# Kernel optimization log

Measured on AMD Instinct MI355X. Metric: run time of the kernel, lower is better.

Reference implementation:

```python
import jax, jax.numpy as jnp
import numpy as np
from jax import lax
from jax.scipy.special import logsumexp

V, H, L, C, B, T = 30000, 512, 2, 9, 128, 256


def setup_inputs() -> dict:
    key = jax.random.key(0)
    ks = jax.random.split(key, 14)
    k = 1.0 / np.sqrt(H)
    u = lambda kk, shp, s: jax.random.uniform(kk, shp, jnp.float32, -s, s)
    embed = jax.random.normal(ks[0], (V, H), jnp.float32) * 0.5
    embed = embed.at[0].set(0.0)  # padding_idx=0
    w_ih_l0 = u(ks[1], (2, 4 * H, H), k)      # [dir, 4H, in]
    w_hh_l0 = u(ks[2], (2, 4 * H, H), k)
    b_l0 = u(ks[3], (2, 4 * H), k)            # b_ih + b_hh combined
    w_ih_l1 = u(ks[4], (2, 4 * H, 2 * H), k)  # layer-1 input is 2H (bidir concat)
    w_hh_l1 = u(ks[5], (2, 4 * H, H), k)
    b_l1 = u(ks[6], (2, 4 * H), k)
    kc = 1.0 / np.sqrt(2 * H)
    cls_w = u(ks[7], (C, 2 * H), kc)
    cls_b = u(ks[8], (C,), kc)
    crf_start = u(ks[9], (C,), 0.1)
    crf_end = u(ks[10], (C,), 0.1)
    crf_trans = u(ks[11], (C, C), 0.1)
    x = jax.random.randint(ks[12], (B, T), 0, V)
    y = jax.random.randint(ks[13], (B, T), 0, C)
    return dict(x=x, y=y, embed=embed, w_ih_l0=w_ih_l0, w_hh_l0=w_hh_l0, b_l0=b_l0,
                w_ih_l1=w_ih_l1, w_hh_l1=w_hh_l1, b_l1=b_l1, cls_w=cls_w, cls_b=cls_b,
                crf_start=crf_start, crf_end=crf_end, crf_trans=crf_trans)


def _lstm_dir(xs, w_ih, w_hh, b):
    # xs: [T, B, Din] -> hidden states [T, B, H]
    Bn, Hn = xs.shape[1], w_hh.shape[-1]
    pre = jnp.einsum('tbd,gd->tbg', xs, w_ih) + b  # hoist input GEMM out of scan

    def step(carry, zt):
        h, c = carry
        z = zt + h @ w_hh.T
        i, f, g, o = jnp.split(z, 4, axis=-1)
        c = jax.nn.sigmoid(f) * c + jax.nn.sigmoid(i) * jnp.tanh(g)
        h = jax.nn.sigmoid(o) * jnp.tanh(c)
        return (h, c), h

    init = (jnp.zeros((Bn, Hn), xs.dtype), jnp.zeros((Bn, Hn), xs.dtype))
    _, hs = lax.scan(step, init, pre)
    return hs


def _bilstm_layer(xs, w_ih, w_hh, b):
    hf = _lstm_dir(xs, w_ih[0], w_hh[0], b[0])
    hb = _lstm_dir(xs[::-1], w_ih[1], w_hh[1], b[1])[::-1]
    return jnp.concatenate([hf, hb], axis=-1)  # [T, B, 2H]


def reference(x, y, embed, w_ih_l0, w_hh_l0, b_l0, w_ih_l1, w_hh_l1, b_l1,
              cls_w, cls_b, crf_start, crf_end, crf_trans):
    mask = y > -1                              # [B, T] (all True here)
    # Embedding with max_norm=1 (rows renormalized to L2 norm <= 1 at lookup)
    emb = embed[x]                             # [B, T, H]
    nrm = jnp.linalg.norm(emb, axis=-1, keepdims=True)
    emb = emb * jnp.where(nrm > 1.0, 1.0 / (nrm + 1e-7), 1.0)

    xs = emb.transpose(1, 0, 2)                # [T, B, H]
    hs = _bilstm_layer(xs, w_ih_l0, w_hh_l0, b_l0)
    hs = _bilstm_layer(hs, w_ih_l1, w_hh_l1, b_l1)
    emissions = jnp.einsum('tbh,ch->tbc', hs, cls_w) + cls_b  # [T, B, C]

    tags = jnp.maximum(y, 0).T                 # [T, B]
    mT = mask.T                                # [T, B] bool
    mF = mT.astype(emissions.dtype)
    bidx = jnp.arange(B)

    # ---- numerator: score of gold path ----
    em_tag = jnp.take_along_axis(emissions, tags[:, :, None], axis=-1)[..., 0]  # [T, B]
    trans_sc = crf_trans[tags[:-1], tags[1:]]  # [T-1, B]
    score = crf_start[tags[0]] + em_tag[0]
    score = score + jnp.sum((trans_sc + em_tag[1:]) * mF[1:], axis=0)
    seq_ends = jnp.sum(mT, axis=0) - 1         # [B]
    last_tags = tags[seq_ends, bidx]
    score = score + crf_end[last_tags]

    # ---- denominator: forward algorithm ----
    alpha0 = crf_start + emissions[0]          # [B, C]

    def den_step(alpha, inp):
        e_t, m_t = inp
        nxt = logsumexp(alpha[:, :, None] + crf_trans[None] + e_t[:, None, :], axis=1)
        return jnp.where(m_t[:, None], nxt, alpha), None

    alpha, _ = lax.scan(den_step, alpha0, (emissions[1:], mT[1:]))
    denom = logsumexp(alpha + crf_end, axis=1)

    llh = score - denom
    return -jnp.mean(llh)
```

## Files before the change

kernel.cpp:

```cpp
#include <hip/hip_runtime.h>
#include <hip/hip_bf16.h>

#define VV 30000
#define HH 512
#define NC 9
#define BB 128
#define TT 256
#define GG 2048
#define TB (TT*BB)

using short8 = __attribute__((ext_vector_type(8))) short;
using f32x4  = __attribute__((ext_vector_type(4))) float;

__device__ inline float bf2f(unsigned short u){
    union { unsigned int i; float f; } v; v.i = ((unsigned int)u) << 16; return v.f;
}
__device__ inline unsigned short f2bf(float f){
    union { unsigned int i; float f; } v; v.f = f;
    unsigned int x = v.i;
    unsigned int r = (x + 0x7fffu + ((x >> 16) & 1u)) >> 16;
    return (unsigned short)r;
}
__device__ inline float sigm(float x){
    if (x >= 0.f){ return 1.f / (1.f + __expf(-x)); }
    float e = __expf(x); return e / (1.f + e);
}
__device__ inline float tanh_f(float x){
    float ax = fabsf(x);
    float e = __expf(-2.f * ax);
    float t = (1.f - e) / (1.f + e);
    return copysignf(t, x);
}

__global__ void castbf(const float* __restrict__ in, unsigned short* __restrict__ out, int n){
    int i = blockIdx.x * blockDim.x + threadIdx.x;
    if (i < n) out[i] = f2bf(in[i]);
}

__global__ __launch_bounds__(256) void embed_k(const int* __restrict__ x,
                                               const float* __restrict__ embed,
                                               unsigned short* __restrict__ xs){
    int wid  = (int)((blockIdx.x * blockDim.x + threadIdx.x) >> 6);
    int lane = threadIdx.x & 63;
    if (wid >= TB) return;
    int t = wid >> 7, b = wid & 127;
    int tok = x[b * TT + t];
    const float4* e = (const float4*)(embed + (size_t)tok * HH);
    float4 v0 = e[lane], v1 = e[lane + 64];
    float ss = v0.x*v0.x + v0.y*v0.y + v0.z*v0.z + v0.w*v0.w
             + v1.x*v1.x + v1.y*v1.y + v1.z*v1.z + v1.w*v1.w;
    #pragma unroll
    for (int off = 32; off > 0; off >>= 1) ss += __shfl_xor(ss, off, 64);
    float nrm = sqrtf(ss);
    float sc = (nrm > 1.f) ? 1.f / (nrm + 1e-7f) : 1.f;
    unsigned short* dst = xs + (size_t)wid * HH;
    ushort4 o0, o1;
    o0.x = f2bf(v0.x * sc); o0.y = f2bf(v0.y * sc); o0.z = f2bf(v0.z * sc); o0.w = f2bf(v0.w * sc);
    o1.x = f2bf(v1.x * sc); o1.y = f2bf(v1.y * sc); o1.z = f2bf(v1.z * sc); o1.w = f2bf(v1.w * sc);
    ((ushort4*)dst)[lane]      = o0;
    ((ushort4*)dst)[lane + 64] = o1;
}

__global__ __launch_bounds__(256) void gemm2(const unsigned short* __restrict__ A0,
                                             const unsigned short* __restrict__ A1,
                                             const unsigned short* __restrict__ Wb_,
                                             const float* __restrict__ bias,
                                             unsigned short* __restrict__ Cout,
                                             int K, int CH){
    const int dz = blockIdx.z;
    const unsigned short* A  = dz ? A1 : A0;
    const unsigned short* W  = Wb_ + (size_t)dz * GG * K;
    const float*          bd = bias + dz * GG;
    unsigned short*       C  = Cout + (size_t)dz * CH * BB * GG;

    __shared__ __align__(16) unsigned short smem[16384];

    const int tid  = threadIdx.x;
    const int lane = tid & 63;
    const int wv   = tid >> 6;
    const int l15  = lane & 15, quad = lane >> 4;
    const int mw   = (wv >> 1) * 64;
    const int nw   = (wv & 1) * 64;

    const int nwg   = gridDim.x * gridDim.y;
    const int chunk = nwg >> 3;
    const int id    = blockIdx.x + gridDim.x * blockIdx.y;
    const int nid   = (id & 7) * chunk + (id >> 3);
    const int m0    = (nid % gridDim.x) * 128;
    const int n0    = (nid / gridDim.x) * 128;

    const int srow = lane >> 2;
    const int scol = (lane & 3) * 8;
    const int c0 = wv * 2, c1 = wv * 2 + 1;
    const unsigned short* gA0 = A + (size_t)(m0 + c0 * 16 + srow) * K + scol;
    const unsigned short* gA1 = A + (size_t)(m0 + c1 * 16 + srow) * K + scol;
    const unsigned short* gB0 = W + (size_t)(n0 + c0 * 16 + srow) * K + scol;
    const unsigned short* gB1 = W + (size_t)(n0 + c1 * 16 + srow) * K + scol;

    f32x4 acc[4][4];
    #pragma unroll
    for (int i = 0; i < 4; i++)
        #pragma unroll
        for (int j = 0; j < 4; j++){ acc[i][j][0]=0.f; acc[i][j][1]=0.f; acc[i][j][2]=0.f; acc[i][j][3]=0.f; }

    #define STAGE(bufi, kko)                                                                              \
        do {                                                                                              \
            __builtin_amdgcn_global_load_lds((const __attribute__((address_space(1))) void*)(gA0 + (kko)),\
                (__attribute__((address_space(3))) void*)(smem + (bufi) * 4096 + c0 * 512), 16, 0, 0);    \
            __builtin_amdgcn_global_load_lds((const __attribute__((address_space(1))) void*)(gA1 + (kko)),\
                (__attribute__((address_space(3))) void*)(smem + (bufi) * 4096 + c1 * 512), 16, 0, 0);    \
            __builtin_amdgcn_global_load_lds((const __attribute__((address_space(1))) void*)(gB0 + (kko)),\
                (__attribute__((address_space(3))) void*)(smem + 8192 + (bufi) * 4096 + c0 * 512), 16, 0, 0);\
            __builtin_amdgcn_global_load_lds((const __attribute__((address_space(1))) void*)(gB1 + (kko)),\
                (__attribute__((address_space(3))) void*)(smem + 8192 + (bufi) * 4096 + c1 * 512), 16, 0, 0);\
        } while (0)

    const int nk = K >> 5;
    STAGE(0, 0);
    for (int t = 0; t < nk; ++t){
        const int buf = t & 1;
        const bool more = (t + 1 < nk);
        if (more){
            STAGE((t + 1) & 1, (t + 1) << 5);
            __builtin_amdgcn_sched_barrier(0);
            asm volatile("s_waitcnt vmcnt(4)" ::: "memory");
        } else {
            __builtin_amdgcn_sched_barrier(0);
            asm volatile("s_waitcnt vmcnt(0)" ::: "memory");
        }
        __builtin_amdgcn_s_barrier();
        __builtin_amdgcn_sched_barrier(0);

        short8 a[4], b[4];
        #pragma unroll
        for (int i = 0; i < 4; i++) a[i] = *(const short8*)&smem[(size_t)buf * 4096 + (mw + i * 16 + l15) * 32 + quad * 8];
        #pragma unroll
        for (int j = 0; j < 4; j++) b[j] = *(const short8*)&smem[8192 + (size_t)buf * 4096 + (nw + j * 16 + l15) * 32 + quad * 8];
        #pragma unroll
        for (int i = 0; i < 4; i++)
            #pragma unroll
            for (int j = 0; j < 4; j++)
                acc[i][j] = __builtin_amdgcn_mfma_f32_16x16x32_bf16(a[i], b[j], acc[i][j], 0, 0, 0);

        __builtin_amdgcn_sched_barrier(0);
        __builtin_amdgcn_s_barrier();
        __builtin_amdgcn_sched_barrier(0);
    }
    #undef STAGE

    #pragma unroll
    for (int i = 0; i < 4; i++){
        #pragma unroll
        for (int j = 0; j < 4; j++){
            const int ncol = nw + j * 16 + l15;
            const float bn = bd[n0 + ncol];
            #pragma unroll
            for (int r = 0; r < 4; r++){
                const int mrow = mw + i * 16 + quad * 4 + r;
                smem[mrow * 128 + ncol] = f2bf(acc[i][j][r] + bn);
            }
        }
    }
    __syncthreads();
    #pragma unroll
    for (int it = 0; it < 8; it++){
        const int ch  = it * 256 + tid;
        const int row = ch >> 4;
        const int col = (ch & 15) * 8;
        *(short8*)(C + (size_t)(m0 + row) * GG + n0 + col) = *(const short8*)&smem[row * 128 + col];
    }
}

__global__ __launch_bounds__(256) void lstm_seq(const unsigned short* __restrict__ preC,
                                                const unsigned short* __restrict__ whh,
                                                unsigned short* __restrict__ hA,
                                                unsigned short* __restrict__ hB,
                                                float* __restrict__ cstate,
                                                unsigned short* __restrict__ hs_out,
                                                const float* __restrict__ cw,
                                                float* __restrict__ em,
                                                int t0, int nsteps, int CH,
                                                unsigned int* __restrict__ bar){
    __shared__ unsigned short w_s[4][16][520];
    __shared__ unsigned short htile[64][20];
    __shared__ float cw_s[NC][16];

    const int tid  = threadIdx.x;
    const int lane = tid & 63;
    const int wv   = tid >> 6;
    const int l15  = lane & 15, quad = lane >> 4;
    const int bx   = blockIdx.x;
    const int grp  = bx & 3;
    const int d    = grp >> 1;
    const int mh   = grp & 1;
    const int jc   = bx >> 2;
    const int m0   = mh * 64;

    {
        const unsigned short* wbase = whh + (size_t)d * GG * HH;
        #pragma unroll
        for (int it = 0; it < 16; it++){
            int idx  = it * 256 + tid;
            int row  = idx >> 6;
            int col8 = idx & 63;
            int g2 = row >> 4, j2 = row & 15;
            short8 v = *(const short8*)(wbase + (size_t)(g2 * 512 + jc * 16 + j2) * HH + col8 * 8);
            *(short8*)&w_s[g2][j2][col8 * 8] = v;
        }
    }
    if (cw != nullptr && tid < NC * 16){
        int c = tid >> 4, j = tid & 15;
        cw_s[c][j] = cw[(size_t)c * 1024 + d * 512 + jc * 16 + j];
    }

    float csreg[4];
    #pragma unroll
    for (int rr = 0; rr < 4; rr++){
        const int gm = m0 + wv * 16 + quad * 4 + rr;
        csreg[rr] = cstate[((size_t)d * BB + gm) * HH + jc * 16 + l15];
    }

    unsigned short pf[4][4];
    {
        const int time0 = d ? (TT - 1 - t0) : t0;
        const int slot0 = time0 & (CH - 1);
        const unsigned short* p0 = preC + (((size_t)(d * CH + slot0)) * BB + (m0 + wv * 16 + quad * 4)) * GG + jc * 16 + l15;
        #pragma unroll
        for (int rr = 0; rr < 4; rr++)
            #pragma unroll
            for (int g = 0; g < 4; g++)
                pf[rr][g] = p0[(size_t)rr * GG + g * 512];
    }
    __syncthreads();

    const size_t slabU = (size_t)grp * 8192;
    unsigned int* myFl  = bar + (((size_t)grp * 4 + wv) * 32 + jc) * 16;
    const unsigned int* pollFl = bar + (((size_t)grp * 4 + wv) * 32 + (lane & 31)) * 16;

    const int rowu = (wv * 16 + l15) * 4 + (quad & 1) * 2;
    const int jq   = quad >> 1;

    unsigned short pfN[4][4];

    for (int ls = 0; ls < nsteps; ls++){
        const int tt   = t0 + ls;
        const unsigned long long* srcU = (const unsigned long long*)((tt & 1) ? hB : hA) + slabU;
        unsigned long long*       dstU = (unsigned long long*)((tt & 1) ? hA : hB) + slabU + (size_t)jc * 256;

        if (ls > 0){
            const unsigned int tgt = (unsigned int)ls;
            while (__hip_atomic_load(pollFl, __ATOMIC_RELAXED, __HIP_MEMORY_SCOPE_AGENT) < tgt)
                __builtin_amdgcn_s_sleep(1);
            __builtin_amdgcn_fence(__ATOMIC_ACQUIRE, "workgroup");
            #pragma unroll
            for (int rr = 0; rr < 4; rr++)
                #pragma unroll
                for (int g = 0; g < 4; g++)
                    pf[rr][g] = pfN[rr][g];
        }

        unsigned long long afr[16][2];
        #pragma unroll
        for (int kk = 0; kk < 16; kk++){
            const unsigned long long* p = srcU + (size_t)(2 * kk + jq) * 256 + rowu;
            afr[kk][0] = __hip_atomic_load(p,     __ATOMIC_RELAXED, __HIP_MEMORY_SCOPE_AGENT);
            afr[kk][1] = __hip_atomic_load(p + 1, __ATOMIC_RELAXED, __HIP_MEMORY_SCOPE_AGENT);
        }

        f32x4 acc[4];
        #pragma unroll
        for (int g = 0; g < 4; g++){ acc[g][0]=0.f; acc[g][1]=0.f; acc[g][2]=0.f; acc[g][3]=0.f; }
        #pragma unroll
        for (int kk = 0; kk < 16; kk++){
            union { unsigned long long u[2]; short8 s; } cv;
            cv.u[0] = afr[kk][0]; cv.u[1] = afr[kk][1];
            const short8 a = cv.s;
            #pragma unroll
            for (int g = 0; g < 4; g++){
                short8 b = *(const short8*)&w_s[g][l15][kk * 32 + quad * 8];
                acc[g] = __builtin_amdgcn_mfma_f32_16x16x32_bf16(a, b, acc[g], 0, 0, 0);
            }
        }

        #pragma unroll
        for (int rr = 0; rr < 4; rr++){
            const int lr = wv * 16 + quad * 4 + rr;
            const float zi = acc[0][rr] + bf2f(pf[rr][0]);
            const float zf = acc[1][rr] + bf2f(pf[rr][1]);
            const float zg = acc[2][rr] + bf2f(pf[rr][2]);
            const float zo = acc[3][rr] + bf2f(pf[rr][3]);
            float cs = sigm(zf) * csreg[rr] + sigm(zi) * tanh_f(zg);
            csreg[rr] = cs;
            htile[lr][l15] = f2bf(sigm(zo) * tanh_f(cs));
        }
        const int trowL = lane >> 2;
        const unsigned long long hv8 = *(const unsigned long long*)&htile[wv * 16 + trowL][(lane & 3) * 4];

        __hip_atomic_store(dstU + wv * 64 + lane, hv8, __ATOMIC_RELAXED, __HIP_MEMORY_SCOPE_AGENT);
        asm volatile("s_waitcnt vmcnt(0)" ::: "memory");
        __hip_atomic_store(myFl, (unsigned int)(ls + 1), __ATOMIC_RELAXED, __HIP_MEMORY_SCOPE_AGENT);

        const int time = d ? (TT - 1 - tt) : tt;
        const bool more = (ls + 1 < nsteps);

        if (more){
            const int tt1 = tt + 1;
            const int time1 = d ? (TT - 1 - tt1) : tt1;
            const int slot1 = time1 & (CH - 1);
            const unsigned short* p1 = preC + (((size_t)(d * CH + slot1)) * BB + (m0 + wv * 16 + quad * 4)) * GG + jc * 16 + l15;
            #pragma unroll
            for (int rr = 0; rr < 4; rr++)
                #pragma unroll
                for (int g = 0; g < 4; g++)
                    pfN[rr][g] = p1[(size_t)rr * GG + g * 512];
        }

        if (cw == nullptr){
            *(unsigned long long*)(hs_out + ((size_t)time * BB + m0 + wv * 16 + trowL) * (2 * HH) + d * HH + jc * 16 + (lane & 3) * 4) = hv8;
        } else {
            const int part = lane & 3;
            float hvv[4];
            #pragma unroll
            for (int k = 0; k < 4; k++) hvv[k] = bf2f((unsigned short)(hv8 >> (16 * k)));
            float p[NC];
            #pragma unroll
            for (int c = 0; c < NC; c++){
                float s = 0.f;
                #pragma unroll
                for (int k = 0; k < 4; k++) s += hvv[k] * cw_s[c][part * 4 + k];
                p[c] = s;
            }
            #pragma unroll
            for (int c = 0; c < NC; c++){
                p[c] += __shfl_xor(p[c], 1, 64);
                p[c] += __shfl_xor(p[c], 2, 64);
            }
            if (part == 0){
                float* emr = em + ((size_t)time * BB + m0 + wv * 16 + trowL) * NC;
                #pragma unroll
                for (int c = 0; c < NC; c++) atomicAdd(emr + c, p[c]);
            }
        }
    }

    #pragma unroll
    for (int rr = 0; rr < 4; rr++){
        const int gm = m0 + wv * 16 + quad * 4 + rr;
        cstate[((size_t)d * BB + gm) * HH + jc * 16 + l15] = csreg[rr];
    }
}

__global__ void eminit(const float* __restrict__ cb, float* __restrict__ em){
    int i = blockIdx.x * blockDim.x + threadIdx.x;
    if (i < TB * NC) em[i] = cb[i % NC];
}

__global__ __launch_bounds__(64) void crf_k(const int* __restrict__ y,
                                            const float* __restrict__ em,
                                            const float* __restrict__ cstart,
                                            const float* __restrict__ cend,
                                            const float* __restrict__ ctr,
                                            float* __restrict__ llh){
    int b = blockIdx.x;
    int lane = threadIdx.x;

    float sp = 0.f; int cnt = 0;
    for (int t = lane; t < TT; t += 64){
        int yt = y[b * TT + t];
        bool mk = (yt > -1);
        cnt += mk ? 1 : 0;
        if (t >= 1 && mk){
            int yp  = y[b * TT + t - 1];
            int tag  = yt > 0 ? yt : 0;
            int tagp = yp > 0 ? yp : 0;
            sp += ctr[tagp * NC + tag] + em[((size_t)t * BB + b) * NC + tag];
        }
    }
    #pragma unroll
    for (int off = 32; off > 0; off >>= 1){
        sp  += __shfl_xor(sp, off, 64);
        cnt += __shfl_xor(cnt, off, 64);
    }

    float trc[NC];
    #pragma unroll
    for (int cc2 = 0; cc2 < NC; cc2++) trc[cc2] = 0.f;
    if (lane < NC){
        #pragma unroll
        for (int cc2 = 0; cc2 < NC; cc2++) trc[cc2] = ctr[cc2 * NC + lane];
    }
    float alpha = -1e30f;
    if (lane < NC) alpha = cstart[lane] + em[(size_t)b * NC + lane];

    for (int t = 1; t < TT; t++){
        int yt = y[b * TT + t];
        bool mk = (yt > -1);
        float e = (lane < NC) ? em[((size_t)t * BB + b) * NC + lane] : 0.f;
        float v[NC]; float mx = -1e30f;
        #pragma unroll
        for (int cc2 = 0; cc2 < NC; cc2++){
            float ac = __shfl(alpha, cc2, 64);
            v[cc2] = ac + trc[cc2];
            mx = fmaxf(mx, v[cc2]);
        }
        float s = 0.f;
        #pragma unroll
        for (int cc2 = 0; cc2 < NC; cc2++) s += __expf(v[cc2] - mx);
        float nxt = mx + __logf(s) + e;
        if (mk && lane < NC) alpha = nxt;
    }

    float val = (lane < NC) ? (alpha + cend[lane]) : -1e30f;
    float mx = -1e30f;
    #pragma unroll
    for (int cc2 = 0; cc2 < NC; cc2++) mx = fmaxf(mx, __shfl(val, cc2, 64));
    float s = 0.f;
    #pragma unroll
    for (int cc2 = 0; cc2 < NC; cc2++) s += __expf(__shfl(val, cc2, 64) - mx);
    float denom = mx + __logf(s);

    if (lane == 0){
        int y0 = y[b * TT];
        int tag0 = y0 > 0 ? y0 : 0;
        int se = cnt - 1;
        if (se < 0) se = 0;
        int yl = y[b * TT + se];
        int tagl = yl > 0 ? yl : 0;
        float score = sp + cstart[tag0] + em[(size_t)b * NC + tag0] + cend[tagl];
        llh[b] = score - denom;
    }
}

__global__ void final_k(const float* __restrict__ llh, float* __restrict__ out){
    __shared__ float sm[128];
    int i = threadIdx.x;
    sm[i] = llh[i];
    __syncthreads();
    for (int s = 64; s > 0; s >>= 1){
        if (i < s) sm[i] += sm[i + s];
        __syncthreads();
    }
    if (i == 0) out[0] = -sm[0] / 128.f;
}

__global__ void sentinel_k(float* out, float v){ out[0] = v; }

extern "C" void kernel_launch(void* const* d_in, const int* in_sizes, int n_in,
                              void* d_out, int out_size, void* d_ws, size_t ws_size,
                              hipStream_t stream) {
    const int*   x     = (const int*)d_in[0];
    const int*   y     = (const int*)d_in[1];
    const float* embed = (const float*)d_in[2];
    const float* wih0  = (const float*)d_in[3];
    const float* whh0  = (const float*)d_in[4];
    const float* b0    = (const float*)d_in[5];
    const float* wih1  = (const float*)d_in[6];
    const float* whh1  = (const float*)d_in[7];
    const float* b1    = (const float*)d_in[8];
    const float* clsw  = (const float*)d_in[9];
    const float* clsb  = (const float*)d_in[10];
    const float* cst   = (const float*)d_in[11];
    const float* cen   = (const float*)d_in[12];
    const float* ctr   = (const float*)d_in[13];
    float* out = (float*)d_out;

    const size_t sz_w0   = (size_t)2 * GG * HH * 2;
    const size_t sz_w1   = (size_t)2 * GG * 1024 * 2;
    const size_t sz_xs   = (size_t)TB * HH * 2;
    const size_t sz_hs0  = (size_t)TB * 1024 * 2;
    const size_t sz_h    = (size_t)2 * BB * HH * 2;
    const size_t sz_c    = (size_t)2 * BB * HH * 4;
    const size_t sz_emis = (size_t)TB * NC * 4;
    const size_t sz_llh  = (size_t)BB * 4;
    const size_t sz_bar  = 32768;
    auto rup = [](size_t v){ return (v + 255) & ~(size_t)255; };
    size_t fixed = rup(sz_w0) * 3 + rup(sz_w1) + rup(sz_xs) + rup(sz_hs0)
                 + rup(sz_h) * 2 + rup(sz_c) + rup(sz_emis) + rup(sz_llh) + rup(sz_bar);

    const int cands[7] = {256, 128, 64, 32, 16, 8, 4};
    int CH = 0;
    for (int i = 0; i < 7; i++){
        size_t need = fixed + rup((size_t)2 * cands[i] * BB * GG * 2);
        if (need <= ws_size){ CH = cands[i]; break; }
    }
    if (CH == 0){
        sentinel_k<<<1, 1, 0, stream>>>(out, -(float)(ws_size >> 20));
        return;
    }

    char* ws = (char*)d_ws;
    size_t off = 0;
    auto alloc = [&](size_t bytes) -> void* {
        void* p = (void*)(ws + off);
        off += (bytes + 255) & ~(size_t)255;
        return p;
    };
    unsigned short* wih0b = (unsigned short*)alloc(sz_w0);
    unsigned short* whh0b = (unsigned short*)alloc(sz_w0);
    unsigned short* whh1b = (unsigned short*)alloc(sz_w0);
    unsigned short* wih1b = (unsigned short*)alloc(sz_w1);
    unsigned short* xs    = (unsigned short*)alloc(sz_xs);
    unsigned short* hs0   = (unsigned short*)alloc(sz_hs0);
    unsigned short* hA    = (unsigned short*)alloc(sz_h);
    unsigned short* hB    = (unsigned short*)alloc(sz_h);
    float*          cbuf  = (float*)alloc(sz_c);
    float*          emis  = (float*)alloc(sz_emis);
    float*          llh   = (float*)alloc(sz_llh);
    unsigned int*   bar   = (unsigned int*)alloc(sz_bar);
    unsigned short* preC  = (unsigned short*)alloc((size_t)2 * CH * BB * GG * 2);

    castbf<<<(2 * GG * HH + 255) / 256, 256, 0, stream>>>(wih0, wih0b, 2 * GG * HH);
    castbf<<<(2 * GG * HH + 255) / 256, 256, 0, stream>>>(whh0, whh0b, 2 * GG * HH);
    castbf<<<(2 * GG * 1024 + 255) / 256, 256, 0, stream>>>(wih1, wih1b, 2 * GG * 1024);
    castbf<<<(2 * GG * HH + 255) / 256, 256, 0, stream>>>(whh1, whh1b, 2 * GG * HH);

    embed_k<<<TB / 4, 256, 0, stream>>>(x, embed, xs);

    const int nch = TT / CH;

    (void)hipMemsetAsync(hA, 0, sz_h, stream);
    (void)hipMemsetAsync(cbuf, 0, sz_c, stream);
    for (int c = 0; c < nch; c++){
        int t0f = c * CH;
        int t0b = TT - (c + 1) * CH;
        gemm2<<<dim3(CH, GG / 128, 2), 256, 0, stream>>>(
            xs + (size_t)t0f * BB * HH, xs + (size_t)t0b * BB * HH,
            wih0b, b0, preC, HH, CH);
        (void)hipMemsetAsync(bar, 0, sz_bar, stream);
        lstm_seq<<<128, 256, 0, stream>>>(preC, whh0b, hA, hB, cbuf, hs0,
                                          nullptr, emis, c * CH, CH, CH, bar);
    }

    eminit<<<(TB * NC + 255) / 256, 256, 0, stream>>>(clsb, emis);

    (void)hipMemsetAsync(hA, 0, sz_h, stream);
    (void)hipMemsetAsync(cbuf, 0, sz_c, stream);
    for (int c = 0; c < nch; c++){
        int t0f = c * CH;
        int t0b = TT - (c + 1) * CH;
        gemm2<<<dim3(CH, GG / 128, 2), 256, 0, stream>>>(
            hs0 + (size_t)t0f * BB * 1024, hs0 + (size_t)t0b * BB * 1024,
            wih1b, b1, preC, 1024, CH);
        (void)hipMemsetAsync(bar, 0, sz_bar, stream);
        lstm_seq<<<128, 256, 0, stream>>>(preC, whh1b, hA, hB, cbuf, hs0,
                                          clsw, emis, c * CH, CH, CH, bar);
    }

    crf_k<<<BB, 64, 0, stream>>>(y, emis, cst, cen, ctr, llh);
    final_k<<<1, 128, 0, stream>>>(llh, out);
}
```

Before: 5.015 ms.

## Overlap next-chunk input GEMM with LSTM recurrence in a fused kernel

```diff
diff --git a/kernel.cpp b/kernel.cpp
--- a/kernel.cpp
+++ b/kernel.cpp
@@ -171,182 +171,300 @@
     }
 }
 
-__global__ __launch_bounds__(256) void lstm_seq(const unsigned short* __restrict__ preC,
-                                                const unsigned short* __restrict__ whh,
-                                                unsigned short* __restrict__ hA,
-                                                unsigned short* __restrict__ hB,
-                                                float* __restrict__ cstate,
-                                                unsigned short* __restrict__ hs_out,
-                                                const float* __restrict__ cw,
-                                                float* __restrict__ em,
-                                                int t0, int nsteps, int CH,
-                                                unsigned int* __restrict__ bar){
-    __shared__ unsigned short w_s[4][16][520];
-    __shared__ unsigned short htile[64][20];
-    __shared__ float cw_s[NC][16];
+__global__ __launch_bounds__(256) void lstm_fused(const unsigned short* __restrict__ preC,
+                                                  const unsigned short* __restrict__ whh,
+                                                  unsigned short* __restrict__ hA,
+                                                  unsigned short* __restrict__ hB,
+                                                  float* __restrict__ cstate,
+                                                  unsigned short* __restrict__ hs_out,
+                                                  const float* __restrict__ cw,
+                                                  float* __restrict__ em,
+                                                  int t0, int nsteps, int CH,
+                                                  unsigned int* __restrict__ bar,
+                                                  const unsigned short* __restrict__ An0,
+                                                  const unsigned short* __restrict__ An1,
+                                                  const unsigned short* __restrict__ Wi_,
+                                                  const float* __restrict__ bias,
+                                                  unsigned short* __restrict__ Cnext,
+                                                  int K, int njobs){
+    __shared__ __align__(16) unsigned char shm[69888];
 
     const int tid  = threadIdx.x;
+    const int bx   = blockIdx.x;
+
+    if (bx < 128){
+        unsigned short (*w_s)[16][520] = (unsigned short (*)[16][520])shm;
+        unsigned short (*htile)[20]    = (unsigned short (*)[20])(shm + 66560);
+        float (*cw_s)[16]              = (float (*)[16])(shm + 69120);
+
+        const int lane = tid & 63;
+        const int wv   = tid >> 6;
+        const int l15  = lane & 15, quad = lane >> 4;
+        const int grp  = bx & 3;
+        const int d    = grp >> 1;
+        const int mh   = grp & 1;
+        const int jc   = bx >> 2;
+        const int m0   = mh * 64;
+
+        {
+            const unsigned short* wbase = whh + (size_t)d * GG * HH;
+            #pragma unroll
+            for (int it = 0; it < 16; it++){
+                int idx  = it * 256 + tid;
+                int row  = idx >> 6;
+                int col8 = idx & 63;
+                int g2 = row >> 4, j2 = row & 15;
+                short8 v = *(const short8*)(wbase + (size_t)(g2 * 512 + jc * 16 + j2) * HH + col8 * 8);
+                *(short8*)&w_s[g2][j2][col8 * 8] = v;
+            }
+        }
+        if (cw != nullptr && tid < NC * 16){
+            int c = tid >> 4, j = tid & 15;
+            cw_s[c][j] = cw[(size_t)c * 1024 + d * 512 + jc * 16 + j];
+        }
+
+        float csreg[4];
+        #pragma unroll
+        for (int rr = 0; rr < 4; rr++){
+            const int gm = m0 + wv * 16 + quad * 4 + rr;
+            csreg[rr] = cstate[((size_t)d * BB + gm) * HH + jc * 16 + l15];
+        }
+
+        unsigned short pf[4][4];
+        {
+            const int time0 = d ? (TT - 1 - t0) : t0;
+            const int slot0 = time0 & (CH - 1);
+            const unsigned short* p0 = preC + (((size_t)(d * CH + slot0)) * BB + (m0 + wv * 16 + quad * 4)) * GG + jc * 16 + l15;
+            #pragma unroll
+            for (int rr = 0; rr < 4; rr++)
+                #pragma unroll
+                for (int g = 0; g < 4; g++)
+                    pf[rr][g] = p0[(size_t)rr * GG + g * 512];
+        }
+        __syncthreads();
+
+        const size_t slabU = (size_t)grp * 8192;
+        unsigned int* myFl  = bar + (((size_t)grp * 4 + wv) * 32 + jc) * 16;
+        const unsigned int* pollFl = bar + (((size_t)grp * 4 + wv) * 32 + (lane & 31)) * 16;
+
+        const int rowu = (wv * 16 + l15) * 4 + (quad & 1) * 2;
+        const int jq   = quad >> 1;
+
+        unsigned short pfN[4][4];
+
+        for (int ls = 0; ls < nsteps; ls++){
+            const int tt   = t0 + ls;
+            const unsigned long long* srcU = (const unsigned long long*)((tt & 1) ? hB : hA) + slabU;
+            unsigned long long*       dstU = (unsigned long long*)((tt & 1) ? hA : hB) + slabU + (size_t)jc * 256;
+
+            if (ls > 0){
+                const unsigned int tgt = (unsigned int)ls;
+                while (__hip_atomic_load(pollFl, __ATOMIC_RELAXED, __HIP_MEMORY_SCOPE_AGENT) < tgt)
+                    __builtin_amdgcn_s_sleep(1);
+                __builtin_amdgcn_fence(__ATOMIC_ACQUIRE, "workgroup");
+                #pragma unroll
+                for (int rr = 0; rr < 4; rr++)
+                    #pragma unroll
+                    for (int g = 0; g < 4; g++)
+                        pf[rr][g] = pfN[rr][g];
+            }
+
+            unsigned long long afr[16][2];
+            #pragma unroll
+            for (int kk = 0; kk < 16; kk++){
+                const unsigned long long* p = srcU + (size_t)(2 * kk + jq) * 256 + rowu;
+                afr[kk][0] = __hip_atomic_load(p,     __ATOMIC_RELAXED, __HIP_MEMORY_SCOPE_AGENT);
+                afr[kk][1] = __hip_atomic_load(p + 1, __ATOMIC_RELAXED, __HIP_MEMORY_SCOPE_AGENT);
+            }
+
+            f32x4 acc[4];
+            #pragma unroll
+            for (int g = 0; g < 4; g++){ acc[g][0]=0.f; acc[g][1]=0.f; acc[g][2]=0.f; acc[g][3]=0.f; }
+            #pragma unroll
+            for (int kk = 0; kk < 16; kk++){
+                union { unsigned long long u[2]; short8 s; } cv;
+                cv.u[0] = afr[kk][0]; cv.u[1] = afr[kk][1];
+                const short8 a = cv.s;
+                #pragma unroll
+                for (int g = 0; g < 4; g++){
+                    short8 b = *(const short8*)&w_s[g][l15][kk * 32 + quad * 8];
+                    acc[g] = __builtin_amdgcn_mfma_f32_16x16x32_bf16(a, b, acc[g], 0, 0, 0);
+                }
+            }
+
+            #pragma unroll
+            for (int rr = 0; rr < 4; rr++){
+                const int lr = wv * 16 + quad * 4 + rr;
+                const float zi = acc[0][rr] + bf2f(pf[rr][0]);
+                const float zf = acc[1][rr] + bf2f(pf[rr][1]);
+                const float zg = acc[2][rr] + bf2f(pf[rr][2]);
+                const float zo = acc[3][rr] + bf2f(pf[rr][3]);
+                float cs = sigm(zf) * csreg[rr] + sigm(zi) * tanh_f(zg);
+                csreg[rr] = cs;
+                htile[lr][l15] = f2bf(sigm(zo) * tanh_f(cs));
+            }
+            const int trowL = lane >> 2;
+            const unsigned long long hv8 = *(const unsigned long long*)&htile[wv * 16 + trowL][(lane & 3) * 4];
+
+            __hip_atomic_store(dstU + wv * 64 + lane, hv8, __ATOMIC_RELAXED, __HIP_MEMORY_SCOPE_AGENT);
+            asm volatile("s_waitcnt vmcnt(0)" ::: "memory");
+            __hip_atomic_store(myFl, (unsigned int)(ls + 1), __ATOMIC_RELAXED, __HIP_MEMORY_SCOPE_AGENT);
+
+            const int time = d ? (TT - 1 - tt) : tt;
+            const bool more = (ls + 1 < nsteps);
+
+            if (more){
+                const int tt1 = tt + 1;
+                const int time1 = d ? (TT - 1 - tt1) : tt1;
+                const int slot1 = time1 & (CH - 1);
+                const unsigned short* p1 = preC + (((size_t)(d * CH + slot1)) * BB + (m0 + wv * 16 + quad * 4)) * GG + jc * 16 + l15;
+                #pragma unroll
+                for (int rr = 0; rr < 4; rr++)
+                    #pragma unroll
+                    for (int g = 0; g < 4; g++)
+                        pfN[rr][g] = p1[(size_t)rr * GG + g * 512];
+            }
+
+            if (cw == nullptr){
+                *(unsigned long long*)(hs_out + ((size_t)time * BB + m0 + wv * 16 + trowL) * (2 * HH) + d * HH + jc * 16 + (lane & 3) * 4) = hv8;
+            } else {
+                const int part = lane & 3;
+                float hvv[4];
+                #pragma unroll
+                for (int k = 0; k < 4; k++) hvv[k] = bf2f((unsigned short)(hv8 >> (16 * k)));
+                float p[NC];
+                #pragma unroll
+                for (int c = 0; c < NC; c++){
+                    float s = 0.f;
+                    #pragma unroll
+                    for (int k = 0; k < 4; k++) s += hvv[k] * cw_s[c][part * 4 + k];
+                    p[c] = s;
+                }
+                #pragma unroll
+                for (int c = 0; c < NC; c++){
+                    p[c] += __shfl_xor(p[c], 1, 64);
+                    p[c] += __shfl_xor(p[c], 2, 64);
+                }
+                if (part == 0){
+                    float* emr = em + ((size_t)time * BB + m0 + wv * 16 + trowL) * NC;
+                    #pragma unroll
+                    for (int c = 0; c < NC; c++) atomicAdd(emr + c, p[c]);
+                }
+            }
+        }
+
+        #pragma unroll
+        for (int rr = 0; rr < 4; rr++){
+            const int gm = m0 + wv * 16 + quad * 4 + rr;
+            cstate[((size_t)d * BB + gm) * HH + jc * 16 + l15] = csreg[rr];
+        }
+        return;
+    }
+
+    if (An0 == nullptr) return;
+    unsigned short* smem = (unsigned short*)shm;
+
     const int lane = tid & 63;
     const int wv   = tid >> 6;
     const int l15  = lane & 15, quad = lane >> 4;
-    const int bx   = blockIdx.x;
-    const int grp  = bx & 3;
-    const int d    = grp >> 1;
-    const int mh   = grp & 1;
-    const int jc   = bx >> 2;
-    const int m0   = mh * 64;
-
-    {
-        const unsigned short* wbase = whh + (size_t)d * GG * HH;
-        #pragma unroll
-        for (int it = 0; it < 16; it++){
-            int idx  = it * 256 + tid;
-            int row  = idx >> 6;
-            int col8 = idx & 63;
-            int g2 = row >> 4, j2 = row & 15;
-            short8 v = *(const short8*)(wbase + (size_t)(g2 * 512 + jc * 16 + j2) * HH + col8 * 8);
-            *(short8*)&w_s[g2][j2][col8 * 8] = v;
-        }
-    }
-    if (cw != nullptr && tid < NC * 16){
-        int c = tid >> 4, j = tid & 15;
-        cw_s[c][j] = cw[(size_t)c * 1024 + d * 512 + jc * 16 + j];
-    }
-
-    float csreg[4];
-    #pragma unroll
-    for (int rr = 0; rr < 4; rr++){
-        const int gm = m0 + wv * 16 + quad * 4 + rr;
-        csreg[rr] = cstate[((size_t)d * BB + gm) * HH + jc * 16 + l15];
-    }
-
-    unsigned short pf[4][4];
-    {
-        const int time0 = d ? (TT - 1 - t0) : t0;
-        const int slot0 = time0 & (CH - 1);
-        const unsigned short* p0 = preC + (((size_t)(d * CH + slot0)) * BB + (m0 + wv * 16 + quad * 4)) * GG + jc * 16 + l15;
-        #pragma unroll
-        for (int rr = 0; rr < 4; rr++)
-            #pragma unroll
-            for (int g = 0; g < 4; g++)
-                pf[rr][g] = p0[(size_t)rr * GG + g * 512];
-    }
-    __syncthreads();
-
-    const size_t slabU = (size_t)grp * 8192;
-    unsigned int* myFl  = bar + (((size_t)grp * 4 + wv) * 32 + jc) * 16;
-    const unsigned int* pollFl = bar + (((size_t)grp * 4 + wv) * 32 + (lane & 31)) * 16;
-
-    const int rowu = (wv * 16 + l15) * 4 + (quad & 1) * 2;
-    const int jq   = quad >> 1;
-
-    unsigned short pfN[4][4];
-
-    for (int ls = 0; ls < nsteps; ls++){
-        const int tt   = t0 + ls;
-        const unsigned long long* srcU = (const unsigned long long*)((tt & 1) ? hB : hA) + slabU;
-        unsigned long long*       dstU = (unsigned long long*)((tt & 1) ? hA : hB) + slabU + (size_t)jc * 256;
-
-        if (ls > 0){
-            const unsigned int tgt = (unsigned int)ls;
-            while (__hip_atomic_load(pollFl, __ATOMIC_RELAXED, __HIP_MEMORY_SCOPE_AGENT) < tgt)
-                __builtin_amdgcn_s_sleep(1);
-            __builtin_amdgcn_fence(__ATOMIC_ACQUIRE, "workgroup");
-            #pragma unroll
-            for (int rr = 0; rr < 4; rr++)
-                #pragma unroll
-                for (int g = 0; g < 4; g++)
-                    pf[rr][g] = pfN[rr][g];
-        }
-
-        unsigned long long afr[16][2];
-        #pragma unroll
-        for (int kk = 0; kk < 16; kk++){
-            const unsigned long long* p = srcU + (size_t)(2 * kk + jq) * 256 + rowu;
-            afr[kk][0] = __hip_atomic_load(p,     __ATOMIC_RELAXED, __HIP_MEMORY_SCOPE_AGENT);
-            afr[kk][1] = __hip_atomic_load(p + 1, __ATOMIC_RELAXED, __HIP_MEMORY_SCOPE_AGENT);
-        }
-
-        f32x4 acc[4];
-        #pragma unroll
-        for (int g = 0; g < 4; g++){ acc[g][0]=0.f; acc[g][1]=0.f; acc[g][2]=0.f; acc[g][3]=0.f; }
-        #pragma unroll
-        for (int kk = 0; kk < 16; kk++){
-            union { unsigned long long u[2]; short8 s; } cv;
-            cv.u[0] = afr[kk][0]; cv.u[1] = afr[kk][1];
-            const short8 a = cv.s;
-            #pragma unroll
-            for (int g = 0; g < 4; g++){
-                short8 b = *(const short8*)&w_s[g][l15][kk * 32 + quad * 8];
-                acc[g] = __builtin_amdgcn_mfma_f32_16x16x32_bf16(a, b, acc[g], 0, 0, 0);
-            }
-        }
-
-        #pragma unroll
-        for (int rr = 0; rr < 4; rr++){
-            const int lr = wv * 16 + quad * 4 + rr;
-            const float zi = acc[0][rr] + bf2f(pf[rr][0]);
-            const float zf = acc[1][rr] + bf2f(pf[rr][1]);
-            const float zg = acc[2][rr] + bf2f(pf[rr][2]);
-            const float zo = acc[3][rr] + bf2f(pf[rr][3]);
-            float cs = sigm(zf) * csreg[rr] + sigm(zi) * tanh_f(zg);
-            csreg[rr] = cs;
-            htile[lr][l15] = f2bf(sigm(zo) * tanh_f(cs));
-        }
-        const int trowL = lane >> 2;
-        const unsigned long long hv8 = *(const unsigned long long*)&htile[wv * 16 + trowL][(lane & 3) * 4];
-
-        __hip_atomic_store(dstU + wv * 64 + lane, hv8, __ATOMIC_RELAXED, __HIP_MEMORY_SCOPE_AGENT);
-        asm volatile("s_waitcnt vmcnt(0)" ::: "memory");
-        __hip_atomic_store(myFl, (unsigned int)(ls + 1), __ATOMIC_RELAXED, __HIP_MEMORY_SCOPE_AGENT);
-
-        const int time = d ? (TT - 1 - tt) : tt;
-        const bool more = (ls + 1 < nsteps);
-
-        if (more){
-            const int tt1 = tt + 1;
-            const int time1 = d ? (TT - 1 - tt1) : tt1;
-            const int slot1 = time1 & (CH - 1);
-            const unsigned short* p1 = preC + (((size_t)(d * CH + slot1)) * BB + (m0 + wv * 16 + quad * 4)) * GG + jc * 16 + l15;
-            #pragma unroll
-            for (int rr = 0; rr < 4; rr++)
-                #pragma unroll
-                for (int g = 0; g < 4; g++)
-                    pfN[rr][g] = p1[(size_t)rr * GG + g * 512];
-        }
-
-        if (cw == nullptr){
-            *(unsigned long long*)(hs_out + ((size_t)time * BB + m0 + wv * 16 + trowL) * (2 * HH) + d * HH + jc * 16 + (lane & 3) * 4) = hv8;
-        } else {
-            const int part = lane & 3;
-            float hvv[4];
-            #pragma unroll
-            for (int k = 0; k < 4; k++) hvv[k] = bf2f((unsigned short)(hv8 >> (16 * k)));
-            float p[NC];
-            #pragma unroll
-            for (int c = 0; c < NC; c++){
-                float s = 0.f;
-                #pragma unroll
-                for (int k = 0; k < 4; k++) s += hvv[k] * cw_s[c][part * 4 + k];
-                p[c] = s;
-            }
-            #pragma unroll
-            for (int c = 0; c < NC; c++){
-                p[c] += __shfl_xor(p[c], 1, 64);
-                p[c] += __shfl_xor(p[c], 2, 64);
-            }
-            if (part == 0){
-                float* emr = em + ((size_t)time * BB + m0 + wv * 16 + trowL) * NC;
-                #pragma unroll
-                for (int c = 0; c < NC; c++) atomicAdd(emr + c, p[c]);
-            }
-        }
-    }
-
-    #pragma unroll
-    for (int rr = 0; rr < 4; rr++){
-        const int gm = m0 + wv * 16 + quad * 4 + rr;
-        cstate[((size_t)d * BB + gm) * HH + jc * 16 + l15] = csreg[rr];
+    const int mw   = (wv >> 1) * 64;
+    const int nw   = (wv & 1) * 64;
+    const int srow = lane >> 2;
+    const int scol = (lane & 3) * 8;
+    const int c0 = wv * 2, c1 = wv * 2 + 1;
+    const int nhb = (int)gridDim.x - 128;
+    const int CHn = nsteps;
+
+    for (int job = bx - 128; job < njobs; job += nhb){
+        const int xj  = job % CHn;
+        const int rem = job / CHn;
+        const int yj  = rem & 15;
+        const int dz  = rem >> 4;
+        const unsigned short* A  = dz ? An1 : An0;
+        const unsigned short* W  = Wi_ + (size_t)dz * GG * K;
+        const float*          bd = bias + dz * GG;
+        unsigned short*       C  = Cnext + (size_t)dz * CHn * BB * GG;
+        const int m0 = xj * 128;
+        const int n0 = yj * 128;
+
+        const unsigned short* gA0 = A + (size_t)(m0 + c0 * 16 + srow) * K + scol;
+        const unsigned short* gA1 = A + (size_t)(m0 + c1 * 16 + srow) * K + scol;
+        const unsigned short* gB0 = W + (size_t)(n0 + c0 * 16 + srow) * K + scol;
+        const unsigned short* gB1 = W + (size_t)(n0 + c1 * 16 + srow) * K + scol;
+
+        f32x4 acc[4][4];
+        #pragma unroll
+        for (int i = 0; i < 4; i++)
+            #pragma unroll
+            for (int j = 0; j < 4; j++){ acc[i][j][0]=0.f; acc[i][j][1]=0.f; acc[i][j][2]=0.f; acc[i][j][3]=0.f; }
+
+        #define HSTAGE(bufi, kko)                                                                             \
+            do {                                                                                              \
+                __builtin_amdgcn_global_load_lds((const __attribute__((address_space(1))) void*)(gA0 + (kko)),\
+                    (__attribute__((address_space(3))) void*)(smem + (bufi) * 4096 + c0 * 512), 16, 0, 0);    \
+                __builtin_amdgcn_global_load_lds((const __attribute__((address_space(1))) void*)(gA1 + (kko)),\
+                    (__attribute__((address_space(3))) void*)(smem + (bufi) * 4096 + c1 * 512), 16, 0, 0);    \
+                __builtin_amdgcn_global_load_lds((const __attribute__((address_space(1))) void*)(gB0 + (kko)),\
+                    (__attribute__((address_space(3))) void*)(smem + 8192 + (bufi) * 4096 + c0 * 512), 16, 0, 0);\
+                __builtin_amdgcn_global_load_lds((const __attribute__((address_space(1))) void*)(gB1 + (kko)),\
+                    (__attribute__((address_space(3))) void*)(smem + 8192 + (bufi) * 4096 + c1 * 512), 16, 0, 0);\
+            } while (0)
+
+        const int nk = K >> 5;
+        HSTAGE(0, 0);
+        for (int t = 0; t < nk; ++t){
+            const int buf = t & 1;
+            const bool more = (t + 1 < nk);
+            if (more){
+                HSTAGE((t + 1) & 1, (t + 1) << 5);
+                __builtin_amdgcn_sched_barrier(0);
+                asm volatile("s_waitcnt vmcnt(4)" ::: "memory");
+            } else {
+                __builtin_amdgcn_sched_barrier(0);
+                asm volatile("s_waitcnt vmcnt(0)" ::: "memory");
+            }
+            __builtin_amdgcn_s_barrier();
+            __builtin_amdgcn_sched_barrier(0);
+
+            short8 a[4], b[4];
+            #pragma unroll
+            for (int i = 0; i < 4; i++) a[i] = *(const short8*)&smem[(size_t)buf * 4096 + (mw + i * 16 + l15) * 32 + quad * 8];
+            #pragma unroll
+            for (int j = 0; j < 4; j++) b[j] = *(const short8*)&smem[8192 + (size_t)buf * 4096 + (nw + j * 16 + l15) * 32 + quad * 8];
+            #pragma unroll
+            for (int i = 0; i < 4; i++)
+                #pragma unroll
+                for (int j = 0; j < 4; j++)
+                    acc[i][j] = __builtin_amdgcn_mfma_f32_16x16x32_bf16(a[i], b[j], acc[i][j], 0, 0, 0);
+
+            __builtin_amdgcn_sched_barrier(0);
+            __builtin_amdgcn_s_barrier();
+            __builtin_amdgcn_sched_barrier(0);
+        }
+        #undef HSTAGE
+
+        #pragma unroll
+        for (int i = 0; i < 4; i++){
+            #pragma unroll
+            for (int j = 0; j < 4; j++){
+                const int ncol = nw + j * 16 + l15;
+                const float bn = bd[n0 + ncol];
+                #pragma unroll
+                for (int r = 0; r < 4; r++){
+                    const int mrow = mw + i * 16 + quad * 4 + r;
+                    smem[mrow * 128 + ncol] = f2bf(acc[i][j][r] + bn);
+                }
+            }
+        }
+        __syncthreads();
+        #pragma unroll
+        for (int it = 0; it < 8; it++){
+            const int ch  = it * 256 + tid;
+            const int row = ch >> 4;
+            const int col = (ch & 15) * 8;
+            *(short8*)(C + (size_t)(m0 + row) * GG + n0 + col) = *(const short8*)&smem[row * 128 + col];
+        }
+        __syncthreads();
     }
 }
 
@@ -477,16 +595,17 @@
     size_t fixed = rup(sz_w0) * 3 + rup(sz_w1) + rup(sz_xs) + rup(sz_hs0)
                  + rup(sz_h) * 2 + rup(sz_c) + rup(sz_emis) + rup(sz_llh) + rup(sz_bar);
 
-    const int cands[7] = {256, 128, 64, 32, 16, 8, 4};
+    const int cands[4] = {64, 32, 16, 8};
     int CH = 0;
-    for (int i = 0; i < 7; i++){
-        size_t need = fixed + rup((size_t)2 * cands[i] * BB * GG * 2);
-        if (need <= ws_size){ CH = cands[i]; break; }
+    for (int i = 0; i < 4; i++){
+        size_t par = (size_t)2 * cands[i] * BB * GG * 2;
+        if (fixed + 2 * rup(par) <= ws_size){ CH = cands[i]; break; }
     }
     if (CH == 0){
         sentinel_k<<<1, 1, 0, stream>>>(out, -(float)(ws_size >> 20));
         return;
     }
+    const size_t parSz = (size_t)2 * CH * BB * GG * 2;
 
     char* ws = (char*)d_ws;
     size_t off = 0;
@@ -507,7 +626,8 @@
     float*          emis  = (float*)alloc(sz_emis);
     float*          llh   = (float*)alloc(sz_llh);
     unsigned int*   bar   = (unsigned int*)alloc(sz_bar);
-    unsigned short* preC  = (unsigned short*)alloc((size_t)2 * CH * BB * GG * 2);
+    unsigned short* preC0 = (unsigned short*)alloc(parSz);
+    unsigned short* preC1 = (unsigned short*)alloc(parSz);
 
     castbf<<<(2 * GG * HH + 255) / 256, 256, 0, stream>>>(wih0, wih0b, 2 * GG * HH);
     castbf<<<(2 * GG * HH + 255) / 256, 256, 0, stream>>>(whh0, whh0b, 2 * GG * HH);
@@ -517,33 +637,40 @@
     embed_k<<<TB / 4, 256, 0, stream>>>(x, embed, xs);
 
     const int nch = TT / CH;
+    const int njobs = CH * 16 * 2;
+
+    eminit<<<(TB * NC + 255) / 256, 256, 0, stream>>>(clsb, emis);
 
     (void)hipMemsetAsync(hA, 0, sz_h, stream);
     (void)hipMemsetAsync(cbuf, 0, sz_c, stream);
+    gemm2<<<dim3(CH, GG / 128, 2), 256, 0, stream>>>(
+        xs, xs + (size_t)(TT - CH) * BB * HH, wih0b, b0, preC0, HH, CH);
     for (int c = 0; c < nch; c++){
-        int t0f = c * CH;
-        int t0b = TT - (c + 1) * CH;
-        gemm2<<<dim3(CH, GG / 128, 2), 256, 0, stream>>>(
-            xs + (size_t)t0f * BB * HH, xs + (size_t)t0b * BB * HH,
-            wih0b, b0, preC, HH, CH);
+        unsigned short* cur = (c & 1) ? preC1 : preC0;
+        unsigned short* nxt = (c & 1) ? preC0 : preC1;
+        const bool more = (c + 1 < nch);
         (void)hipMemsetAsync(bar, 0, sz_bar, stream);
-        lstm_seq<<<128, 256, 0, stream>>>(preC, whh0b, hA, hB, cbuf, hs0,
-                                          nullptr, emis, c * CH, CH, CH, bar);
-    }
-
-    eminit<<<(TB * NC + 255) / 256, 256, 0, stream>>>(clsb, emis);
+        lstm_fused<<<384, 256, 0, stream>>>(cur, whh0b, hA, hB, cbuf, hs0,
+            nullptr, emis, c * CH, CH, CH, bar,
+            more ? xs + (size_t)(c + 1) * CH * BB * HH : nullptr,
+            more ? xs + (size_t)(TT - (size_t)(c + 2) * CH) * BB * HH : nullptr,
+            wih0b, b0, nxt, HH, njobs);
+    }
 
     (void)hipMemsetAsync(hA, 0, sz_h, stream);
     (void)hipMemsetAsync(cbuf, 0, sz_c, stream);
+    gemm2<<<dim3(CH, GG / 128, 2), 256, 0, stream>>>(
+        hs0, hs0 + (size_t)(TT - CH) * BB * 1024, wih1b, b1, preC0, 1024, CH);
     for (int c = 0; c < nch; c++){
-        int t0f = c * CH;
-        int t0b = TT - (c + 1) * CH;
-        gemm2<<<dim3(CH, GG / 128, 2), 256, 0, stream>>>(
-            hs0 + (size_t)t0f * BB * 1024, hs0 + (size_t)t0b * BB * 1024,
-            wih1b, b1, preC, 1024, CH);
+        unsigned short* cur = (c & 1) ? preC1 : preC0;
+        unsigned short* nxt = (c & 1) ? preC0 : preC1;
+        const bool more = (c + 1 < nch);
         (void)hipMemsetAsync(bar, 0, sz_bar, stream);
-        lstm_seq<<<128, 256, 0, stream>>>(preC, whh1b, hA, hB, cbuf, hs0,
-                                          clsw, emis, c * CH, CH, CH, bar);
+        lstm_fused<<<384, 256, 0, stream>>>(cur, whh1b, hA, hB, cbuf, hs0,
+            clsw, emis, c * CH, CH, CH, bar,
+            more ? hs0 + (size_t)(c + 1) * CH * BB * 1024 : nullptr,
+            more ? hs0 + (size_t)(TT - (size_t)(c + 2) * CH) * BB * 1024 : nullptr,
+            wih1b, b1, nxt, 1024, njobs);
     }
 
     crf_k<<<BB, 64, 0, stream>>>(y, emis, cst, cen, ctr, llh);
```

New measurement: 4.694 ms. -6.4%, faster.
